# Kernel optimization log

Measured on AMD Instinct MI355X. Metric: run time of the kernel, lower is better.

Reference implementation:

```python
import jax, jax.numpy as jnp
import numpy as np

NUM_IMUS = 13
NUM_PARAMS = 9
EPS = 1e-5
LN_EPS = 1e-5


def setup_inputs() -> dict:
    key = jax.random.key(0)
    k1, k2, k3 = jax.random.split(key, 3)
    d_model, S = 512, 2048
    hidden_states = jax.random.normal(k1, (1, S, d_model), dtype=jnp.float32)
    min_orig_accel_norm = jax.random.normal(k2, (1,), dtype=jnp.float32)
    W = jax.random.normal(k3, (d_model, NUM_IMUS * NUM_PARAMS), dtype=jnp.float32) * 0.02
    b = jnp.zeros((NUM_IMUS * NUM_PARAMS,), jnp.float32)
    ln_w = jnp.ones((d_model,), jnp.float32)
    ln_b = jnp.zeros((d_model,), jnp.float32)
    return {"hidden_states": hidden_states, "min_orig_accel_norm": min_orig_accel_norm,
            "ln_w": ln_w, "ln_b": ln_b, "W": W, "b": b}


def _layernorm(x, w, bias):
    mu = x.mean(-1, keepdims=True)
    var = ((x - mu) ** 2).mean(-1, keepdims=True)
    return (x - mu) * jax.lax.rsqrt(var + LN_EPS) * w + bias


def reference(hidden_states, min_orig_accel_norm, ln_w, ln_b, W, b):
    S = hidden_states.shape[1]
    x = _layernorm(hidden_states, ln_w, ln_b)
    # (1,S,117) -> (S, 9, 13); batch is always 1
    p = (x @ W + b).reshape(S, NUM_PARAMS, NUM_IMUS)
    c, c_th, phi, phi_th = p[:, 4], p[:, 5], p[:, 6], p[:, 7]  # (S,13) each
    d = jnp.sqrt(p[:, 1] ** 2 + EPS)                 # (S,13)
    k = d ** 2 / 4 + jax.nn.softplus(p[:, 0])
    d_th = jnp.sqrt(p[:, 3] ** 2 + EPS)
    k_th = d_th ** 2 / 4 + jax.nn.softplus(p[:, 2])
    noise_bias = p[:, 8].T                           # (13,S)
    om = jnp.sqrt(4 * k - d ** 2) / 2                # = sqrt(softplus(p0))
    om_th = jnp.sqrt(4 * k_th - d_th ** 2) / 2
    t = jnp.arange(S, dtype=jnp.float32)
    tstep = jnp.triu(t[None, :] - t[:, None])        # (S,S), entry (i,j)=j-i for j>=i
    ts = tstep[:, :, None]                           # (S,S,1)

    def src(a):  # params indexed by source step i, broadcast over target step j
        return a[:, None, :]                         # (S,1,13)

    lin = src(c) * jnp.exp(-src(d) / 2 * ts) * jnp.sin(ts * src(om) + src(phi))
    ang = src(c_th) * jnp.exp(-src(d_th) / 2 * ts) * jnp.sin(ts * src(om_th) + src(phi_th))
    mask = jnp.triu(jnp.ones((S, S), jnp.float32))[:, :, None]
    summed = ((lin + ang) * mask).sum(axis=0)        # (S,13): sum over source i<=j
    return summed.T + min_orig_accel_norm + noise_bias  # (13,S)
```

## Files before the change

### kernel.cpp

```cpp
#include <hip/hip_runtime.h>
#include <math.h>

#define S_LEN 2048
#define D_MODEL 512
#define NIMU 13
#define NCOL 117
#define CPAD 128
#define NKC 8
#define KCSTRIDE ((size_t)CPAD * S_LEN)

static __device__ __forceinline__ float softplus_f(float x) {
    return (x > 20.f) ? x : log1pf(expf(x));
}

static __device__ __forceinline__ void osc_init(float pk, float pd, float amp, float phi, float dtf,
                                                float& re, float& im, float& zr, float& zi)
{
    const float LOG2E = 1.4426950408889634f;
    const float INV2PI = 0.15915494309189535f;
    float d = sqrtf(pd * pd + 1e-5f);
    float kk = d * d * 0.25f + softplus_f(pk);
    float om = 0.5f * sqrtf(fmaxf(4.f * kk - d * d, 0.f));
    float y = -0.5f * d * LOG2E;
    float f = om * INV2PI;
    float ph = phi * INV2PI;
    float ez = __builtin_amdgcn_exp2f(y);
    zr = ez * __builtin_amdgcn_cosf(f);
    zi = ez * __builtin_amdgcn_sinf(f);
    float er = amp * __builtin_amdgcn_exp2f(dtf * y);
    float r = fmaf(dtf, f, ph); r -= floorf(r);
    re = er * __builtin_amdgcn_cosf(r);
    im = er * __builtin_amdgcn_sinf(r);
}

__global__ __launch_bounds__(256) void stats_kernel(const float* __restrict__ H,
                                                    float2* __restrict__ stats,
                                                    const float* __restrict__ W,
                                                    float* __restrict__ Wp,
                                                    float* __restrict__ out) {
    if (blockIdx.x < 104) out[blockIdx.x * 256 + threadIdx.x] = 0.f;
    if (threadIdx.x < CPAD) {
        int c = threadIdx.x;
        Wp[blockIdx.x * CPAD + c] = (c < NCOL) ? W[blockIdx.x * NCOL + c] : 0.f;
    }
    int wave = threadIdx.x >> 6;
    int lane = threadIdx.x & 63;
    int row = blockIdx.x * 4 + wave;
    const float* hr = H + row * D_MODEL;
    float4 a = *(const float4*)&hr[lane * 4];
    float4 b = *(const float4*)&hr[256 + lane * 4];
    float sum = a.x + a.y + a.z + a.w + b.x + b.y + b.z + b.w;
    #pragma unroll
    for (int off = 32; off; off >>= 1) sum += __shfl_down(sum, off);
    sum = __shfl(sum, 0);
    float mu = sum * (1.f / 512.f);
    float vs = 0.f;
    vs += (a.x - mu) * (a.x - mu); vs += (a.y - mu) * (a.y - mu);
    vs += (a.z - mu) * (a.z - mu); vs += (a.w - mu) * (a.w - mu);
    vs += (b.x - mu) * (b.x - mu); vs += (b.y - mu) * (b.y - mu);
    vs += (b.z - mu) * (b.z - mu); vs += (b.w - mu) * (b.w - mu);
    #pragma unroll
    for (int off = 32; off; off >>= 1) vs += __shfl_down(vs, off);
    if (lane == 0) {
        float var = vs * (1.f / 512.f);
        stats[row] = make_float2(mu, 1.0f / sqrtf(var + 1e-5f));
    }
}

__global__ __launch_bounds__(128) void proj_kernel(
    const float* __restrict__ H, const float2* __restrict__ stats,
    const float* __restrict__ lnw, const float* __restrict__ lnb,
    const float* __restrict__ Wp, float* __restrict__ Pt)
{
    __shared__ float Xt[64 * 32];
    __shared__ float Ws[64 * CPAD];
    int tid = threadIdx.x;
    int row0 = blockIdx.x * 32;
    int k0 = blockIdx.y * 64;

    {
        const float4* Wp4 = (const float4*)(Wp + k0 * CPAD);
        float4* Ws4 = (float4*)Ws;
        #pragma unroll
        for (int i = 0; i < 16; ++i) Ws4[tid + i * 128] = Wp4[tid + i * 128];
    }
    {
        int r = tid >> 2, fq = tid & 3;
        int row = row0 + r;
        float2 st = stats[row];
        const float4* H4 = (const float4*)(H + row * D_MODEL + k0);
        const float4* w4 = (const float4*)(lnw + k0);
        const float4* b4 = (const float4*)(lnb + k0);
        #pragma unroll
        for (int it = 0; it < 4; ++it) {
            int q = fq + it * 4;
            float4 h = H4[q], wv = w4[q], bv = b4[q];
            Xt[(4 * q + 0) * 32 + r] = (h.x - st.x) * st.y * wv.x + bv.x;
            Xt[(4 * q + 1) * 32 + r] = (h.y - st.x) * st.y * wv.y + bv.y;
            Xt[(4 * q + 2) * 32 + r] = (h.z - st.x) * st.y * wv.z + bv.z;
            Xt[(4 * q + 3) * 32 + r] = (h.w - st.x) * st.y * wv.w + bv.w;
        }
    }
    __syncthreads();

    int q8 = tid & 15;
    int rg = tid >> 4;
    float acc[4][8];
    #pragma unroll
    for (int a = 0; a < 4; ++a)
        for (int u = 0; u < 8; ++u) acc[a][u] = 0.f;

    #pragma unroll 4
    for (int k = 0; k < 64; ++k) {
        float4 xa = *(float4*)&Xt[k * 32 + 4 * rg];
        float4 w0 = *(float4*)&Ws[k * CPAD + 8 * q8];
        float4 w1 = *(float4*)&Ws[k * CPAD + 8 * q8 + 4];
        float xv[4] = {xa.x, xa.y, xa.z, xa.w};
        float wv[8] = {w0.x, w0.y, w0.z, w0.w, w1.x, w1.y, w1.z, w1.w};
        #pragma unroll
        for (int a = 0; a < 4; ++a)
            #pragma unroll
            for (int u = 0; u < 8; ++u)
                acc[a][u] = fmaf(xv[a], wv[u], acc[a][u]);
    }

    if (q8 < 15) {
        #pragma unroll
        for (int u = 0; u < 8; ++u) {
            int c = 8 * q8 + u;
            if (c < NCOL) {
                float4 v = make_float4(acc[0][u], acc[1][u], acc[2][u], acc[3][u]);
                *(float4*)&Pt[((size_t)blockIdx.y * CPAD + c) * S_LEN + row0 + 4 * rg] = v;
            }
        }
    }
}

__global__ __launch_bounds__(256) void main_kernel(
    const float* __restrict__ Pt, const float* __restrict__ bias,
    const float* __restrict__ minp, float* __restrict__ out)
{
    __shared__ float buf[4 * 256];
    int tid = threadIdx.x;
    int lane = tid & 63, w = tid >> 6;
    int m = blockIdx.y;
    int bx = blockIdx.x;

    int g = 0, base = 0;
    #pragma unroll 1
    for (;;) {
        int nb = (g + 4) >> 2;
        if (bx < base + nb) break;
        base += nb; ++g;
    }
    int sub = bx - base;
    int q = sub * 4 + w;

    float* accW = buf + w * 256;
    accW[lane] = 0.f; accW[lane + 64] = 0.f;
    accW[lane + 128] = 0.f; accW[lane + 192] = 0.f;
    __builtin_amdgcn_wave_barrier();

    if (q <= g) {
        int sc = q, tc = g - q;
        int i0 = sc * 128;
        float dtf = (float)(tc * 128);

        float pvA[9], pvB[9];
        #pragma unroll
        for (int p = 0; p < 9; ++p) {
            int c = p * 13 + m;
            const float* bp = Pt + (size_t)c * S_LEN + i0 + lane;
            float vA = bias[c], vB = vA;
            #pragma unroll
            for (int kc = 0; kc < NKC; ++kc) {
                vA += bp[kc * KCSTRIDE];
                vB += bp[kc * KCSTRIDE + 64];
            }
            pvA[p] = vA; pvB[p] = vB;
        }

        float reLA, imLA, zrLA, ziLA; osc_init(pvA[0], pvA[1], pvA[4], pvA[6], dtf, reLA, imLA, zrLA, ziLA);
        float reAA, imAA, zrAA, ziAA; osc_init(pvA[2], pvA[3], pvA[5], pvA[7], dtf, reAA, imAA, zrAA, ziAA);
        float reLB, imLB, zrLB, ziLB; osc_init(pvB[0], pvB[1], pvB[4], pvB[6], dtf, reLB, imLB, zrLB, ziLB);
        float reAB, imAB, zrAB, ziAB; osc_init(pvB[2], pvB[3], pvB[5], pvB[7], dtf, reAB, imAB, zrAB, ziAB);

        #pragma unroll 8
        for (int t = 0; t < 128; ++t) {
            float a0 = accW[lane + t];
            float a1 = accW[lane + 64 + t];
            a0 += imLA + imAA;
            a1 += imLB + imAB;
            accW[lane + t] = a0;
            accW[lane + 64 + t] = a1;
            __builtin_amdgcn_wave_barrier();
            float tL = imLA * ziLA; float rL = fmaf(reLA, zrLA, -tL);
            imLA = fmaf(reLA, ziLA, imLA * zrLA); reLA = rL;
            float tA = imAA * ziAA; float rA = fmaf(reAA, zrAA, -tA);
            imAA = fmaf(reAA, ziAA, imAA * zrAA); reAA = rA;
            float tLB = imLB * ziLB; float rLB = fmaf(reLB, zrLB, -tLB);
            imLB = fmaf(reLB, ziLB, imLB * zrLB); reLB = rLB;
            float tAB = imAB * ziAB; float rAB = fmaf(reAB, zrAB, -tAB);
            imAB = fmaf(reAB, ziAB, imAB * zrAB); reAB = rAB;
        }
    }
    __syncthreads();

    {
        int j = g * 128 + tid;
        if (j < S_LEN) {
            float s = buf[tid] + buf[256 + tid] + buf[512 + tid] + buf[768 + tid];
            if (sub == 0 && tid < 128) {
                int c8 = 8 * 13 + m;
                float v = minp[0] + bias[c8];
                const float* bp = Pt + (size_t)c8 * S_LEN + j;
                #pragma unroll
                for (int kc = 0; kc < NKC; ++kc) v += bp[kc * KCSTRIDE];
                s += v;
            }
            atomicAdd(&out[m * S_LEN + j], s);
        }
    }
}

extern "C" void kernel_launch(void* const* d_in, const int* in_sizes, int n_in,
                              void* d_out, int out_size, void* d_ws, size_t ws_size,
                              hipStream_t stream)
{
    const float* H    = (const float*)d_in[0];
    const float* MINP = (const float*)d_in[1];
    const float* LNW  = (const float*)d_in[2];
    const float* LNB  = (const float*)d_in[3];
    const float* W    = (const float*)d_in[4];
    const float* B    = (const float*)d_in[5];
    float* out = (float*)d_out;

    const size_t PTSZ = (size_t)NKC * CPAD * S_LEN * sizeof(float);
    const size_t STSZ = S_LEN * sizeof(float2);

    char* ws = (char*)d_ws;
    float*  Pt    = (float*)ws;
    float2* stats = (float2*)(ws + PTSZ);
    float*  Wp    = (float*)(ws + PTSZ + STSZ);

    stats_kernel<<<512, 256, 0, stream>>>(H, stats, W, Wp, out);
    proj_kernel<<<dim3(64, 8), 128, 0, stream>>>(H, stats, LNW, LNB, Wp, Pt);
    main_kernel<<<dim3(40, NIMU), 256, 0, stream>>>(Pt, B, MINP, out);
}
```

Measured before the change: 98.33 us.

## Fuse layernorm statistics and weight padding into the projection kernel

After: 114.1 us. +16.0%, slower.

```diff
diff --git a/kernel.cpp b/kernel.cpp
--- a/kernel.cpp
+++ b/kernel.cpp
@@ -33,44 +33,11 @@
     im = er * __builtin_amdgcn_sinf(r);
 }
 
-__global__ __launch_bounds__(256) void stats_kernel(const float* __restrict__ H,
-                                                    float2* __restrict__ stats,
-                                                    const float* __restrict__ W,
-                                                    float* __restrict__ Wp,
-                                                    float* __restrict__ out) {
-    if (blockIdx.x < 104) out[blockIdx.x * 256 + threadIdx.x] = 0.f;
-    if (threadIdx.x < CPAD) {
-        int c = threadIdx.x;
-        Wp[blockIdx.x * CPAD + c] = (c < NCOL) ? W[blockIdx.x * NCOL + c] : 0.f;
-    }
-    int wave = threadIdx.x >> 6;
-    int lane = threadIdx.x & 63;
-    int row = blockIdx.x * 4 + wave;
-    const float* hr = H + row * D_MODEL;
-    float4 a = *(const float4*)&hr[lane * 4];
-    float4 b = *(const float4*)&hr[256 + lane * 4];
-    float sum = a.x + a.y + a.z + a.w + b.x + b.y + b.z + b.w;
-    #pragma unroll
-    for (int off = 32; off; off >>= 1) sum += __shfl_down(sum, off);
-    sum = __shfl(sum, 0);
-    float mu = sum * (1.f / 512.f);
-    float vs = 0.f;
-    vs += (a.x - mu) * (a.x - mu); vs += (a.y - mu) * (a.y - mu);
-    vs += (a.z - mu) * (a.z - mu); vs += (a.w - mu) * (a.w - mu);
-    vs += (b.x - mu) * (b.x - mu); vs += (b.y - mu) * (b.y - mu);
-    vs += (b.z - mu) * (b.z - mu); vs += (b.w - mu) * (b.w - mu);
-    #pragma unroll
-    for (int off = 32; off; off >>= 1) vs += __shfl_down(vs, off);
-    if (lane == 0) {
-        float var = vs * (1.f / 512.f);
-        stats[row] = make_float2(mu, 1.0f / sqrtf(var + 1e-5f));
-    }
-}
-
 __global__ __launch_bounds__(128) void proj_kernel(
-    const float* __restrict__ H, const float2* __restrict__ stats,
+    const float* __restrict__ H,
     const float* __restrict__ lnw, const float* __restrict__ lnb,
-    const float* __restrict__ Wp, float* __restrict__ Pt)
+    const float* __restrict__ W, float* __restrict__ Pt,
+    float* __restrict__ out)
 {
     __shared__ float Xt[64 * 32];
     __shared__ float Ws[64 * CPAD];
@@ -78,27 +45,51 @@
     int row0 = blockIdx.x * 32;
     int k0 = blockIdx.y * 64;
 
-    {
-        const float4* Wp4 = (const float4*)(Wp + k0 * CPAD);
-        float4* Ws4 = (float4*)Ws;
-        #pragma unroll
-        for (int i = 0; i < 16; ++i) Ws4[tid + i * 128] = Wp4[tid + i * 128];
-    }
-    {
-        int r = tid >> 2, fq = tid & 3;
+    if (blockIdx.y == 0 && tid < 104) {
+        ((float4*)out)[blockIdx.x * 104 + tid] = make_float4(0.f, 0.f, 0.f, 0.f);
+    }
+
+    int r = tid >> 2;
+    int fq = tid & 3;
+    float mu, rstd;
+    {
+        const float4* hq = (const float4*)(H + (size_t)(row0 + r) * D_MODEL + fq * 128);
+        float sum = 0.f, sq = 0.f;
+        #pragma unroll 8
+        for (int i = 0; i < 32; ++i) {
+            float4 v = hq[i];
+            sum += v.x + v.y + v.z + v.w;
+            sq = fmaf(v.x, v.x, fmaf(v.y, v.y, fmaf(v.z, v.z, fmaf(v.w, v.w, sq))));
+        }
+        sum += __shfl_xor(sum, 1); sq += __shfl_xor(sq, 1);
+        sum += __shfl_xor(sum, 2); sq += __shfl_xor(sq, 2);
+        mu = sum * (1.f / 512.f);
+        float var = fmaxf(sq * (1.f / 512.f) - mu * mu, 0.f);
+        rstd = 1.0f / sqrtf(var + 1e-5f);
+    }
+
+    {
+        #pragma unroll 8
+        for (int i = 0; i < 64; ++i) {
+            int idx = tid + i * 128;
+            int k = idx >> 7;
+            int c = idx & 127;
+            Ws[idx] = (c < NCOL) ? W[(size_t)(k0 + k) * NCOL + c] : 0.f;
+        }
+    }
+    {
         int row = row0 + r;
-        float2 st = stats[row];
-        const float4* H4 = (const float4*)(H + row * D_MODEL + k0);
+        const float4* H4 = (const float4*)(H + (size_t)row * D_MODEL + k0);
         const float4* w4 = (const float4*)(lnw + k0);
         const float4* b4 = (const float4*)(lnb + k0);
         #pragma unroll
         for (int it = 0; it < 4; ++it) {
             int q = fq + it * 4;
             float4 h = H4[q], wv = w4[q], bv = b4[q];
-            Xt[(4 * q + 0) * 32 + r] = (h.x - st.x) * st.y * wv.x + bv.x;
-            Xt[(4 * q + 1) * 32 + r] = (h.y - st.x) * st.y * wv.y + bv.y;
-            Xt[(4 * q + 2) * 32 + r] = (h.z - st.x) * st.y * wv.z + bv.z;
-            Xt[(4 * q + 3) * 32 + r] = (h.w - st.x) * st.y * wv.w + bv.w;
+            Xt[(4 * q + 0) * 32 + r] = (h.x - mu) * rstd * wv.x + bv.x;
+            Xt[(4 * q + 1) * 32 + r] = (h.y - mu) * rstd * wv.y + bv.y;
+            Xt[(4 * q + 2) * 32 + r] = (h.z - mu) * rstd * wv.z + bv.z;
+            Xt[(4 * q + 3) * 32 + r] = (h.w - mu) * rstd * wv.w + bv.w;
         }
     }
     __syncthreads();
@@ -235,15 +226,8 @@
     const float* B    = (const float*)d_in[5];
     float* out = (float*)d_out;
 
-    const size_t PTSZ = (size_t)NKC * CPAD * S_LEN * sizeof(float);
-    const size_t STSZ = S_LEN * sizeof(float2);
-
-    char* ws = (char*)d_ws;
-    float*  Pt    = (float*)ws;
-    float2* stats = (float2*)(ws + PTSZ);
-    float*  Wp    = (float*)(ws + PTSZ + STSZ);
-
-    stats_kernel<<<512, 256, 0, stream>>>(H, stats, W, Wp, out);
-    proj_kernel<<<dim3(64, 8), 128, 0, stream>>>(H, stats, LNW, LNB, Wp, Pt);
+    float* Pt = (float*)d_ws;
+
+    proj_kernel<<<dim3(64, 8), 128, 0, stream>>>(H, LNW, LNB, W, Pt, out);
     main_kernel<<<dim3(40, NIMU), 256, 0, stream>>>(Pt, B, MINP, out);
 }
```
